# Kernel tuning notes

Measured on AMD Instinct MI355X. Metric: run time of the kernel, lower is better.

The kernel has to match this reference:

```python
import jax, jax.numpy as jnp
import numpy as np
from jax import lax

B, CIN, IMG, K = 128, 3, 112, 7
C = 1024      # hidden_channels * channel_dilation
HID = 512     # hidden_channels
HW = (IMG // K) ** 2  # 256 patches
EPS = 1e-5


def _prelu(x, a):
    return jnp.where(x > 0, x, a * x)


def _bn(x, g, b):
    # BatchNorm2d with track_running_stats=False: always uses batch stats
    m = x.mean(axis=(0, 2, 3), keepdims=True)
    v = x.var(axis=(0, 2, 3), keepdims=True)
    return (x - m) * lax.rsqrt(v + EPS) * g[None, :, None, None] + b[None, :, None, None]


def setup_inputs() -> dict:
    key = jax.random.key(0)
    ks = jax.random.split(key, 16)
    d = {
        'x':  jax.random.normal(ks[0], (B, CIN, IMG, IMG), jnp.float32),
        'w0': jax.random.normal(ks[1], (C, CIN, K, K), jnp.float32) * 0.05,
        'b0': jax.random.normal(ks[2], (C,), jnp.float32) * 0.01,
        'a0': jnp.full((1,), 0.25, jnp.float32),
    }
    for i in range(1, 4):
        kw, kb = jax.random.split(jax.random.fold_in(key, i))
        d[f'w{i}'] = jax.random.normal(kw, (C, C), jnp.float32) * 0.02
        d[f'b{i}'] = jax.random.normal(kb, (C,), jnp.float32) * 0.01
        d[f'g{i}'] = jnp.ones((C,), jnp.float32)
        d[f'bt{i}'] = jnp.zeros((C,), jnp.float32)
        d[f'p{i}'] = jnp.full((1,), 0.25, jnp.float32)
    d['pos'] = jax.random.normal(ks[3], (1, HW, C), jnp.float32)
    d['am'] = jnp.full((1,), 0.25, jnp.float32)
    d['wm'] = jax.random.normal(ks[4], (HID, C), jnp.float32) * 0.03
    d['bm'] = jax.random.normal(ks[5], (HID,), jnp.float32) * 0.01
    pkeys = jax.random.split(ks[6], B)
    d['perm'] = jax.vmap(lambda k: jax.random.permutation(k, HW))(pkeys).astype(jnp.int32)
    return d


def reference(x, w0, b0, a0,
              w1, b1, g1, bt1, p1,
              w2, b2, g2, bt2, p2,
              w3, b3, g3, bt3, p3,
              pos, am, wm, bm, perm):
    # patch-embed conv: stride = kernel_size -> [B, C, 16, 16]
    h = lax.conv_general_dilated(x, w0, (K, K), 'VALID',
                                 dimension_numbers=('NCHW', 'OIHW', 'NCHW'))
    h = _prelu(h + b0[None, :, None, None], a0)
    for w, b, g, bt, p in ((w1, b1, g1, bt1, p1),
                           (w2, b2, g2, bt2, p2),
                           (w3, b3, g3, bt3, p3)):
        h = jnp.einsum('bchw,dc->bdhw', h, w) + b[None, :, None, None]  # 1x1 conv
        h = _prelu(_bn(h, g, bt), p)
    Bn, Cn, Hn, Wn = h.shape
    enc = h.reshape(Bn, Cn, Hn * Wn).transpose(0, 2, 1)  # [B, HW, C]
    enc = enc + pos                                      # private: add pos embedding
    enc = _prelu(enc, am) @ wm.T + bm                    # mixer -> [B, HW, HID]
    # private: per-sample token permutation (single batched gather)
    return jnp.take_along_axis(enc, perm[:, :, None], axis=1)
```

## Files before the change

### kernel.cpp

```cpp
#include <hip/hip_runtime.h>
#include <hip/hip_bf16.h>
#include <stdint.h>


typedef __attribute__((ext_vector_type(8))) short bf16x8;
typedef __attribute__((ext_vector_type(4))) float f32x4;

__device__ __forceinline__ float bf2f(uint32_t u) {
  union { uint32_t i; float f; } v; v.i = u << 16; return v.f;
}
__device__ __forceinline__ ushort f2bf(float f) {
  union { float f; uint32_t i; } v; v.f = f;
  uint32_t i = v.i;
  return (ushort)((i + 0x7FFFu + ((i >> 16) & 1u)) >> 16);
}

template<int EPI, int XB, int K, int DOUT>
__global__ void __launch_bounds__(512, 2)
gemm_kernel(const ushort* __restrict__ A, const ushort* __restrict__ Bw,
            const float* __restrict__ bias, const float* __restrict__ alpha,
            void* __restrict__ outp, float* __restrict__ part,
            const int* __restrict__ inv)
{
  __shared__ __align__(16) ushort At[2][256 * 64];
  __shared__ __align__(16) ushort Bt[2][256 * 64];
  const int tid  = threadIdx.x;
  const int lane = tid & 63;
  const int wid  = tid >> 6;
  const int wm   = wid >> 2;
  const int wn   = wid & 3;

  const int s = blockIdx.x;
  const int j = s >> 3;
  const int x = j & ((1 << XB) - 1);
  const int y = ((j >> XB) << 3) | (s & 7);
  const int t0 = y << 8;
  const int d0 = x << 8;

  f32x4 acc[8][4] = {};

  const int swz = (((lane >> 4) ^ (lane & 7)) << 4);
  const char* LA0 = (const char*)&At[0][0] + ((((wm << 7) + (lane & 15))) << 7) + swz;
  const char* LA1 = (const char*)&At[0][0] + ((((wm << 7) + (lane & 15))) << 7) + (swz ^ 64);
  const char* LB0 = (const char*)&Bt[0][0] + ((((wn << 6) + (lane & 15))) << 7) + swz;
  const char* LB1 = (const char*)&Bt[0][0] + ((((wn << 6) + (lane & 15))) << 7) + (swz ^ 64);

  const int lrow8 = lane >> 3;
  const int csrc  = (lane & 7) ^ lrow8;
  const ushort* gAw = A  + (size_t)(t0 + (wid << 4) + lrow8) * K + (csrc << 3);
  const ushort* gBw = Bw + (size_t)(d0 + (wid << 4) + lrow8) * K + (csrc << 3);
  char* stA = (char*)&At[0][0] + (wid << 11);
  char* stB = (char*)&Bt[0][0] + (wid << 11);

#define STAGE_A(T, BUF, H) do {                                                          \
    __builtin_amdgcn_global_load_lds(                                                    \
      (const __attribute__((address_space(1))) uint32_t*)(gAw + (size_t)((H)*128)*K + ((size_t)(T) << 6)),     \
      (__attribute__((address_space(3))) uint32_t*)(stA + (BUF)*32768 + (H)*16384), 16, 0, 0);                  \
    __builtin_amdgcn_global_load_lds(                                                    \
      (const __attribute__((address_space(1))) uint32_t*)(gAw + (size_t)((H)*128+8)*K + ((size_t)(T) << 6)),   \
      (__attribute__((address_space(3))) uint32_t*)(stA + (BUF)*32768 + (H)*16384 + 1024), 16, 0, 0);           \
  } while (0)
#define STAGE_B(T, BUF, H) do {                                                          \
    __builtin_amdgcn_global_load_lds(                                                    \
      (const __attribute__((address_space(1))) uint32_t*)(gBw + (size_t)((H)*128)*K + ((size_t)(T) << 6)),     \
      (__attribute__((address_space(3))) uint32_t*)(stB + (BUF)*32768 + (H)*16384), 16, 0, 0);                  \
    __builtin_amdgcn_global_load_lds(                                                    \
      (const __attribute__((address_space(1))) uint32_t*)(gBw + (size_t)((H)*128+8)*K + ((size_t)(T) << 6)),   \
      (__attribute__((address_space(3))) uint32_t*)(stB + (BUF)*32768 + (H)*16384 + 1024), 16, 0, 0);           \
  } while (0)

#define RD_A(dst, BASE, CUR, MH) do {                                                    \
    dst[0] = *(const bf16x8*)((BASE) + (CUR)*32768 + (MH)*8192 + 0);                     \
    dst[1] = *(const bf16x8*)((BASE) + (CUR)*32768 + (MH)*8192 + 2048);                  \
    dst[2] = *(const bf16x8*)((BASE) + (CUR)*32768 + (MH)*8192 + 4096);                  \
    dst[3] = *(const bf16x8*)((BASE) + (CUR)*32768 + (MH)*8192 + 6144);                  \
  } while (0)
#define RD_B(dst, BASE, CUR) do {                                                        \
    dst[0] = *(const bf16x8*)((BASE) + (CUR)*32768 + 0);                                 \
    dst[1] = *(const bf16x8*)((BASE) + (CUR)*32768 + 2048);                              \
    dst[2] = *(const bf16x8*)((BASE) + (CUR)*32768 + 4096);                              \
    dst[3] = *(const bf16x8*)((BASE) + (CUR)*32768 + 6144);                              \
  } while (0)
#define MFMA16(AF, BF, MH) do {                                                          \
    __builtin_amdgcn_s_setprio(1);                                                       \
    _Pragma("unroll")                                                                    \
    for (int m_ = 0; m_ < 4; ++m_)                                                       \
      _Pragma("unroll")                                                                  \
      for (int n_ = 0; n_ < 4; ++n_)                                                     \
        acc[((MH) << 2) + m_][n_] = __builtin_amdgcn_mfma_f32_16x16x32_bf16(             \
            AF[m_], BF[n_], acc[((MH) << 2) + m_][n_], 0, 0, 0);                         \
    __builtin_amdgcn_s_setprio(0);                                                       \
  } while (0)

#define TILE_BODY(T, CUR, HN1, HN2) do {                                                 \
                               \
    if (HN1) { asm volatile("s_waitcnt vmcnt(4)" ::: "memory"); }                        \
    else     { asm volatile("s_waitcnt vmcnt(0)" ::: "memory"); }                        \
    __builtin_amdgcn_s_barrier();                                                        \
                                                                                \
    RD_A(aX, LA0, CUR, 0);                                                               \
    RD_B(b0f, LB0, CUR);                                                                 \
    if (HN1) { STAGE_A((T) + 1, (CUR) ^ 1, 0); STAGE_A((T) + 1, (CUR) ^ 1, 1); }         \
    MFMA16(aX, b0f, 0);                                                                  \
                                                                                \
    RD_A(aY, LA0, CUR, 1);                                                               \
    MFMA16(aY, b0f, 1);                                                                  \
                                                                                \
    RD_A(aX, LA1, CUR, 0);                                                               \
    RD_B(b1f, LB1, CUR);                                                                 \
    MFMA16(aX, b1f, 0);                                                                  \
                       \
    __builtin_amdgcn_s_barrier();                                                        \
    if (HN2) { STAGE_B((T) + 2, CUR, 0); STAGE_B((T) + 2, CUR, 1); }                     \
                                  \
    RD_A(aY, LA1, CUR, 1);                                                               \
    MFMA16(aY, b1f, 1);                                                                  \
  } while (0)

  constexpr int NT = K >> 6;

  STAGE_A(0, 0, 0); STAGE_A(0, 0, 1);
  STAGE_B(0, 0, 0); STAGE_B(0, 0, 1);
  STAGE_B(1, 1, 0); STAGE_B(1, 1, 1);

  bf16x8 aX[4], aY[4], b0f[4], b1f[4];

#pragma unroll 1
  for (int tp = 0; tp < NT; tp += 2) {
    const bool m1 = (tp + 2 < NT);
    TILE_BODY(tp,     0, true, m1);
    TILE_BODY(tp + 1, 1, m1, m1);
  }

  float bs[4];
#pragma unroll
  for (int n = 0; n < 4; ++n) bs[n] = bias[d0 + (wn << 6) + (n << 4) + (lane & 15)];
  float a0v = (EPI == 0) ? alpha[0] : 0.0f;
  float sA[4] = {0.f, 0.f, 0.f, 0.f}, s2A[4] = {0.f, 0.f, 0.f, 0.f};

#pragma unroll
  for (int m = 0; m < 8; ++m) {
#pragma unroll
    for (int r = 0; r < 4; ++r) {
      int row = t0 + (wm << 7) + (m << 4) + ((lane >> 4) << 2) + r;
      int orow = (EPI == 2) ? ((row & ~255) | inv[row]) : row;
#pragma unroll
      for (int n = 0; n < 4; ++n) {
        int d = d0 + (wn << 6) + (n << 4) + (lane & 15);
        float v = acc[m][n][r] + bs[n];
        if (EPI == 0) v = v > 0.f ? v : a0v * v;
        if (EPI == 1) { sA[n] += v; s2A[n] += v * v; }
        if (EPI == 2) ((float*)outp)[(size_t)orow * DOUT + d] = v;
        else          ((ushort*)outp)[(size_t)row * DOUT + d] = f2bf(v);
      }
    }
  }

  if (EPI == 1) {
    float2* sm = (float2*)&At[0][0];
    int slot = (wm << 2) | (lane >> 4);
    __syncthreads();
#pragma unroll
    for (int n = 0; n < 4; ++n) {
      int c = (wn << 6) + (n << 4) + (lane & 15);
      sm[slot * 256 + c] = make_float2(sA[n], s2A[n]);
    }
    __syncthreads();
    if (tid < 256) {
      float ss = 0.f, ss2 = 0.f;
      for (int q = 0; q < 8; ++q) {
        float2 v = sm[q * 256 + tid];
        ss += v.x; ss2 += v.y;
      }
      part[(size_t)y * 2048 + d0 + tid]        = ss;
      part[(size_t)y * 2048 + 1024 + d0 + tid] = ss2;
    }
  }
#undef STAGE_A
#undef STAGE_B
#undef RD_A
#undef RD_B
#undef MFMA16
#undef TILE_BODY
}

__global__ void bnfold_kernel(const float* __restrict__ part, const float* __restrict__ g,
                              const float* __restrict__ bt, float* __restrict__ scsh) {
  int d = (blockIdx.x << 8) + threadIdx.x;
  float s = 0.f, s2 = 0.f;
  for (int j = 0; j < 128; ++j) { s += part[j * 2048 + d]; s2 += part[j * 2048 + 1024 + d]; }
  float mean = s * (1.f / 32768.f);
  float var  = s2 * (1.f / 32768.f) - mean * mean;
  float sc = g[d] * rsqrtf(var + 1e-5f);
  scsh[d] = sc;
  scsh[1024 + d] = bt[d] - mean * sc;
}

template<bool MIX>
__global__ void bnact_kernel(ushort* __restrict__ Y, const float* __restrict__ scsh,
                             const float* __restrict__ p, const float* __restrict__ pos,
                             const float* __restrict__ am) {
  size_t i = (((size_t)blockIdx.x << 8) + threadIdx.x) << 3;
  int d = (int)(i & 1023);
  float pp = p[0];
  float aa = MIX ? am[0] : 0.f;
  float pv[8];
  if (MIX) {
    int prow = (int)((i >> 10) & 255);
    const float4* pb = (const float4*)(pos + ((size_t)prow << 10) + d);
    float4 pA = pb[0], pB = pb[1];
    pv[0]=pA.x; pv[1]=pA.y; pv[2]=pA.z; pv[3]=pA.w;
    pv[4]=pB.x; pv[5]=pB.y; pv[6]=pB.z; pv[7]=pB.w;
  }
  uint4 raw = *(const uint4*)(Y + i);
  uint32_t w[4] = {raw.x, raw.y, raw.z, raw.w};
  uint32_t o[4];
#pragma unroll
  for (int q = 0; q < 4; ++q) {
    int dd = d + q * 2;
    float v0 = bf2f(w[q] & 0xFFFFu) * scsh[dd]     + scsh[1024 + dd];
    float v1 = bf2f(w[q] >> 16)     * scsh[dd + 1] + scsh[1024 + dd + 1];
    v0 = v0 > 0.f ? v0 : pp * v0;
    v1 = v1 > 0.f ? v1 : pp * v1;
    if (MIX) {
      v0 += pv[2 * q];     v1 += pv[2 * q + 1];
      v0 = v0 > 0.f ? v0 : aa * v0;
      v1 = v1 > 0.f ? v1 : aa * v1;
    }
    o[q] = (uint32_t)f2bf(v0) | ((uint32_t)f2bf(v1) << 16);
  }
  *(uint4*)(Y + i) = make_uint4(o[0], o[1], o[2], o[3]);
}

__global__ void invperm_kernel(const int* __restrict__ perm, int* __restrict__ inv) {
  int t = (blockIdx.x << 8) + threadIdx.x;
  inv[(t & ~255) + perm[t]] = t & 255;
}

__global__ void f2b_kernel(const float* __restrict__ in, ushort* __restrict__ out, int n) {
  int i = (blockIdx.x << 8) + threadIdx.x;
  if (i < n) out[i] = f2bf(in[i]);
}

__global__ void padw0_kernel(const float* __restrict__ w0, ushort* __restrict__ o) {
  int d = blockIdx.x, j = threadIdx.x;
  o[d * 256 + j] = (j < 147) ? f2bf(w0[d * 147 + j]) : (ushort)0;
}

__global__ void im2col_kernel(const float* __restrict__ x, ushort* __restrict__ P) {
  int t = blockIdx.x;
  int j = threadIdx.x;
  ushort v = 0;
  if (j < 147) {
    int b = t >> 8, pidx = t & 255;
    int pi = pidx >> 4, pj = pidx & 15;
    int cin = j / 49, rem = j - cin * 49;
    int dy = rem / 7, dx = rem - dy * 7;
    v = f2bf(x[(size_t)(b * 3 + cin) * 12544 + (size_t)(pi * 7 + dy) * 112 + (pj * 7 + dx)]);
  }
  P[(size_t)t * 256 + j] = v;
}

extern "C" void kernel_launch(void* const* d_in, const int* in_sizes, int n_in,
                              void* d_out, int out_size, void* d_ws, size_t ws_size,
                              hipStream_t stream) {
  const float* x   = (const float*)d_in[0];
  const float* w0  = (const float*)d_in[1];
  const float* b0  = (const float*)d_in[2];
  const float* a0  = (const float*)d_in[3];
  const float* w1  = (const float*)d_in[4];
  const float* b1  = (const float*)d_in[5];
  const float* g1  = (const float*)d_in[6];
  const float* bt1 = (const float*)d_in[7];
  const float* p1  = (const float*)d_in[8];
  const float* w2  = (const float*)d_in[9];
  const float* b2  = (const float*)d_in[10];
  const float* g2  = (const float*)d_in[11];
  const float* bt2 = (const float*)d_in[12];
  const float* p2  = (const float*)d_in[13];
  const float* w3  = (const float*)d_in[14];
  const float* b3  = (const float*)d_in[15];
  const float* g3  = (const float*)d_in[16];
  const float* bt3 = (const float*)d_in[17];
  const float* p3  = (const float*)d_in[18];
  const float* pos = (const float*)d_in[19];
  const float* am  = (const float*)d_in[20];
  const float* wm  = (const float*)d_in[21];
  const float* bm  = (const float*)d_in[22];
  const int*  perm = (const int*)d_in[23];

  char* ws = (char*)d_ws;
  ushort* B0   = (ushort*)ws;
  ushort* B1   = (ushort*)(ws + 67108864);
  float*  part = (float*)(ws + 134217728);
  float*  scsh = (float*)(ws + 134217728 + 2097152);
  int*    inv  = (int*)  (ws + 134217728 + 2097152 + 8192);
  ushort* wbuf = (ushort*)(ws + 134217728 + 2097152 + 8192 + 131072);

  invperm_kernel<<<dim3(128), dim3(256), 0, stream>>>(perm, inv);
  im2col_kernel<<<dim3(32768), dim3(256), 0, stream>>>(x, B1);
  padw0_kernel<<<dim3(1024), dim3(256), 0, stream>>>(w0, wbuf);

  gemm_kernel<0, 2, 256, 1024><<<dim3(512), dim3(512), 0, stream>>>(
      B1, wbuf, b0, a0, (void*)B0, nullptr, nullptr);

  f2b_kernel<<<dim3(4096), dim3(256), 0, stream>>>(w1, wbuf, 1048576);
  gemm_kernel<1, 2, 1024, 1024><<<dim3(512), dim3(512), 0, stream>>>(
      B0, wbuf, b1, nullptr, (void*)B1, part, nullptr);
  bnfold_kernel<<<dim3(4), dim3(256), 0, stream>>>(part, g1, bt1, scsh);
  bnact_kernel<false><<<dim3(16384), dim3(256), 0, stream>>>(B1, scsh, p1, nullptr, nullptr);

  f2b_kernel<<<dim3(4096), dim3(256), 0, stream>>>(w2, wbuf, 1048576);
  gemm_kernel<1, 2, 1024, 1024><<<dim3(512), dim3(512), 0, stream>>>(
      B1, wbuf, b2, nullptr, (void*)B0, part, nullptr);
  bnfold_kernel<<<dim3(4), dim3(256), 0, stream>>>(part, g2, bt2, scsh);
  bnact_kernel<false><<<dim3(16384), dim3(256), 0, stream>>>(B0, scsh, p2, nullptr, nullptr);

  f2b_kernel<<<dim3(4096), dim3(256), 0, stream>>>(w3, wbuf, 1048576);
  gemm_kernel<1, 2, 1024, 1024><<<dim3(512), dim3(512), 0, stream>>>(
      B0, wbuf, b3, nullptr, (void*)B1, part, nullptr);
  bnfold_kernel<<<dim3(4), dim3(256), 0, stream>>>(part, g3, bt3, scsh);
  bnact_kernel<true><<<dim3(16384), dim3(256), 0, stream>>>(B1, scsh, p3, pos, am);

  f2b_kernel<<<dim3(2048), dim3(256), 0, stream>>>(wm, wbuf, 524288);
  gemm_kernel<2, 1, 1024, 512><<<dim3(256), dim3(512), 0, stream>>>(
      B1, wbuf, bm, nullptr, d_out, nullptr, inv);
}
```

Before: 394.2 us.

## Fuse BatchNorm apply and PReLU into the next GEMM's A-operand load

Removes the three standalone bnact passes and instead applies the BN scale/shift, PReLU, and (for the last layer) the positional add and mixer PReLU while loading the A tile of the following GEMM. A tiles now go global→registers→transform→LDS instead of direct global_load_lds. This saves a full read and write of the 64MB bf16 activation per layer. In exchange it adds VGPR pressure, per-element ALU inside the GEMM main loop, and extra waitcnt synchronisation that can stall the MFMA pipeline.

```diff
diff --git a/kernel.cpp b/kernel.cpp
--- a/kernel.cpp
+++ b/kernel.cpp
@@ -15,12 +15,33 @@
   return (ushort)((i + 0x7FFFu + ((i >> 16) & 1u)) >> 16);
 }
 
-template<int EPI, int XB, int K, int DOUT>
+template<int PRE>
+__device__ __forceinline__ bf16x8 bnproc(bf16x8 r, float4 sc0, float4 sc1,
+                                         float4 sh0, float4 sh1,
+                                         float4 pv0, float4 pv1,
+                                         float pp, float aa) {
+  float sca[8] = {sc0.x, sc0.y, sc0.z, sc0.w, sc1.x, sc1.y, sc1.z, sc1.w};
+  float sha[8] = {sh0.x, sh0.y, sh0.z, sh0.w, sh1.x, sh1.y, sh1.z, sh1.w};
+  float pva[8] = {pv0.x, pv0.y, pv0.z, pv0.w, pv1.x, pv1.y, pv1.z, pv1.w};
+  bf16x8 o;
+#pragma unroll
+  for (int j = 0; j < 8; ++j) {
+    float v = bf2f((uint32_t)(ushort)r[j]) * sca[j] + sha[j];
+    v = v > 0.f ? v : pp * v;
+    if (PRE == 2) { v += pva[j]; v = v > 0.f ? v : aa * v; }
+    o[j] = (short)f2bf(v);
+  }
+  return o;
+}
+
+template<int EPI, int PRE, int XB, int K, int DOUT>
 __global__ void __launch_bounds__(512, 2)
 gemm_kernel(const ushort* __restrict__ A, const ushort* __restrict__ Bw,
             const float* __restrict__ bias, const float* __restrict__ alpha,
             void* __restrict__ outp, float* __restrict__ part,
-            const int* __restrict__ inv)
+            const int* __restrict__ inv, const float* __restrict__ scshp,
+            const float* __restrict__ pA, const float* __restrict__ posp,
+            const float* __restrict__ pam)
 {
   __shared__ __align__(16) ushort At[2][256 * 64];
   __shared__ __align__(16) ushort Bt[2][256 * 64];
@@ -47,10 +68,19 @@
 
   const int lrow8 = lane >> 3;
   const int csrc  = (lane & 7) ^ lrow8;
-  const ushort* gAw = A  + (size_t)(t0 + (wid << 4) + lrow8) * K + (csrc << 3);
-  const ushort* gBw = Bw + (size_t)(d0 + (wid << 4) + lrow8) * K + (csrc << 3);
-  char* stA = (char*)&At[0][0] + (wid << 11);
-  char* stB = (char*)&Bt[0][0] + (wid << 11);
+  const int kq    = csrc << 3;
+  const int rbase = (wid << 4) + lrow8;
+  const ushort* gAw = A  + (size_t)(t0 + rbase) * K + kq;
+  const ushort* gBw = Bw + (size_t)(d0 + rbase) * K + kq;
+  char* stA  = (char*)&At[0][0] + (wid << 11);
+  char* stB  = (char*)&Bt[0][0] + (wid << 11);
+  char* stAw = (char*)&At[0][0] + (wid << 11) + (lane << 4);
+
+  float ppA = (PRE >= 1) ? pA[0]  : 0.f;
+  float aaM = (PRE == 2) ? pam[0] : 0.f;
+
+  bf16x8 ar0, ar1, ar2, ar3;
+  float4 sc0_, sc1_, sh0_, sh1_;
 
 #define STAGE_A(T, BUF, H) do {                                                          \
     __builtin_amdgcn_global_load_lds(                                                    \
@@ -67,6 +97,48 @@
     __builtin_amdgcn_global_load_lds(                                                    \
       (const __attribute__((address_space(1))) uint32_t*)(gBw + (size_t)((H)*128+8)*K + ((size_t)(T) << 6)),   \
       (__attribute__((address_space(3))) uint32_t*)(stB + (BUF)*32768 + (H)*16384 + 1024), 16, 0, 0);           \
+  } while (0)
+
+#define ISSUE_A_REG(T) do {                                                              \
+    const ushort* pa_ = gAw + ((size_t)(T) << 6);                                        \
+    ar0 = *(const bf16x8*)(pa_);                                                         \
+    ar1 = *(const bf16x8*)(pa_ + (size_t)8 * K);                                         \
+    ar2 = *(const bf16x8*)(pa_ + (size_t)128 * K);                                       \
+    ar3 = *(const bf16x8*)(pa_ + (size_t)136 * K);                                       \
+    const float* sp_ = scshp + ((T) << 6) + kq;                                          \
+    sc0_ = *(const float4*)(sp_);        sc1_ = *(const float4*)(sp_ + 4);               \
+    sh0_ = *(const float4*)(sp_ + 1024); sh1_ = *(const float4*)(sp_ + 1028);            \
+  } while (0)
+
+#define WRITE_A_REG(T, BUF) do {                                                         \
+    bf16x8 w0_, w1_, w2_, w3_;                                                           \
+    if constexpr (PRE == 2) {                                                            \
+      const float* pb_ = posp + ((T) << 6) + kq;                                         \
+      float4 q00 = *(const float4*)(pb_ + (size_t)(rbase      ) * 1024);                 \
+      float4 q01 = *(const float4*)(pb_ + (size_t)(rbase      ) * 1024 + 4);             \
+      float4 q10 = *(const float4*)(pb_ + (size_t)(rbase +   8) * 1024);                 \
+      float4 q11 = *(const float4*)(pb_ + (size_t)(rbase +   8) * 1024 + 4);             \
+      float4 q20 = *(const float4*)(pb_ + (size_t)(rbase + 128) * 1024);                 \
+      float4 q21 = *(const float4*)(pb_ + (size_t)(rbase + 128) * 1024 + 4);             \
+      float4 q30 = *(const float4*)(pb_ + (size_t)(rbase + 136) * 1024);                 \
+      float4 q31 = *(const float4*)(pb_ + (size_t)(rbase + 136) * 1024 + 4);             \
+      w0_ = bnproc<2>(ar0, sc0_, sc1_, sh0_, sh1_, q00, q01, ppA, aaM);                  \
+      w1_ = bnproc<2>(ar1, sc0_, sc1_, sh0_, sh1_, q10, q11, ppA, aaM);                  \
+      w2_ = bnproc<2>(ar2, sc0_, sc1_, sh0_, sh1_, q20, q21, ppA, aaM);                  \
+      w3_ = bnproc<2>(ar3, sc0_, sc1_, sh0_, sh1_, q30, q31, ppA, aaM);                  \
+    } else {                                                                             \
+      float4 z_ = make_float4(0.f, 0.f, 0.f, 0.f);                                       \
+      w0_ = bnproc<1>(ar0, sc0_, sc1_, sh0_, sh1_, z_, z_, ppA, 0.f);                    \
+      w1_ = bnproc<1>(ar1, sc0_, sc1_, sh0_, sh1_, z_, z_, ppA, 0.f);                    \
+      w2_ = bnproc<1>(ar2, sc0_, sc1_, sh0_, sh1_, z_, z_, ppA, 0.f);                    \
+      w3_ = bnproc<1>(ar3, sc0_, sc1_, sh0_, sh1_, z_, z_, ppA, 0.f);                    \
+    }                                                                                    \
+    char* d_ = stAw + (BUF) * 32768;                                                     \
+    *(bf16x8*)(d_ + 0)     = w0_;                                                        \
+    *(bf16x8*)(d_ + 1024)  = w1_;                                                        \
+    *(bf16x8*)(d_ + 16384) = w2_;                                                        \
+    *(bf16x8*)(d_ + 17408) = w3_;                                                        \
+    asm volatile("s_waitcnt lgkmcnt(0)" ::: "memory");                                   \
   } while (0)
 
 #define RD_A(dst, BASE, CUR, MH) do {                                                    \
@@ -93,14 +165,16 @@
   } while (0)
 
 #define TILE_BODY(T, CUR, HN1, HN2) do {                                                 \
-                               \
     if (HN1) { asm volatile("s_waitcnt vmcnt(4)" ::: "memory"); }                        \
     else     { asm volatile("s_waitcnt vmcnt(0)" ::: "memory"); }                        \
     __builtin_amdgcn_s_barrier();                                                        \
                                                                                 \
     RD_A(aX, LA0, CUR, 0);                                                               \
     RD_B(b0f, LB0, CUR);                                                                 \
-    if (HN1) { STAGE_A((T) + 1, (CUR) ^ 1, 0); STAGE_A((T) + 1, (CUR) ^ 1, 1); }         \
+    if (HN1) {                                                                           \
+      if constexpr (PRE == 0) { STAGE_A((T) + 1, (CUR) ^ 1, 0); STAGE_A((T) + 1, (CUR) ^ 1, 1); } \
+      else ISSUE_A_REG((T) + 1);                                                         \
+    }                                                                                    \
     MFMA16(aX, b0f, 0);                                                                  \
                                                                                 \
     RD_A(aY, LA0, CUR, 1);                                                               \
@@ -109,17 +183,28 @@
     RD_A(aX, LA1, CUR, 0);                                                               \
     RD_B(b1f, LB1, CUR);                                                                 \
     MFMA16(aX, b1f, 0);                                                                  \
-                       \
+                                       \
     __builtin_amdgcn_s_barrier();                                                        \
     if (HN2) { STAGE_B((T) + 2, CUR, 0); STAGE_B((T) + 2, CUR, 1); }                     \
-                                  \
+    if constexpr (PRE >= 1) {                                                            \
+      if (HN2)      { asm volatile("s_waitcnt vmcnt(4)" ::: "memory"); }                 \
+      else if (HN1) { asm volatile("s_waitcnt vmcnt(0)" ::: "memory"); }                 \
+      if (HN1) WRITE_A_REG((T) + 1, (CUR) ^ 1);                                          \
+    }                                                                                    \
+                                                                                \
     RD_A(aY, LA1, CUR, 1);                                                               \
     MFMA16(aY, b1f, 1);                                                                  \
   } while (0)
 
   constexpr int NT = K >> 6;
 
-  STAGE_A(0, 0, 0); STAGE_A(0, 0, 1);
+  if constexpr (PRE == 0) {
+    STAGE_A(0, 0, 0); STAGE_A(0, 0, 1);
+  } else {
+    ISSUE_A_REG(0);
+    asm volatile("s_waitcnt vmcnt(0)" ::: "memory");
+    WRITE_A_REG(0, 0);
+  }
   STAGE_B(0, 0, 0); STAGE_B(0, 0, 1);
   STAGE_B(1, 1, 0); STAGE_B(1, 1, 1);
 
@@ -178,6 +263,8 @@
   }
 #undef STAGE_A
 #undef STAGE_B
+#undef ISSUE_A_REG
+#undef WRITE_A_REG
 #undef RD_A
 #undef RD_B
 #undef MFMA16
@@ -194,42 +281,6 @@
   float sc = g[d] * rsqrtf(var + 1e-5f);
   scsh[d] = sc;
   scsh[1024 + d] = bt[d] - mean * sc;
-}
-
-template<bool MIX>
-__global__ void bnact_kernel(ushort* __restrict__ Y, const float* __restrict__ scsh,
-                             const float* __restrict__ p, const float* __restrict__ pos,
-                             const float* __restrict__ am) {
-  size_t i = (((size_t)blockIdx.x << 8) + threadIdx.x) << 3;
-  int d = (int)(i & 1023);
-  float pp = p[0];
-  float aa = MIX ? am[0] : 0.f;
-  float pv[8];
-  if (MIX) {
-    int prow = (int)((i >> 10) & 255);
-    const float4* pb = (const float4*)(pos + ((size_t)prow << 10) + d);
-    float4 pA = pb[0], pB = pb[1];
-    pv[0]=pA.x; pv[1]=pA.y; pv[2]=pA.z; pv[3]=pA.w;
-    pv[4]=pB.x; pv[5]=pB.y; pv[6]=pB.z; pv[7]=pB.w;
-  }
-  uint4 raw = *(const uint4*)(Y + i);
-  uint32_t w[4] = {raw.x, raw.y, raw.z, raw.w};
-  uint32_t o[4];
-#pragma unroll
-  for (int q = 0; q < 4; ++q) {
-    int dd = d + q * 2;
-    float v0 = bf2f(w[q] & 0xFFFFu) * scsh[dd]     + scsh[1024 + dd];
-    float v1 = bf2f(w[q] >> 16)     * scsh[dd + 1] + scsh[1024 + dd + 1];
-    v0 = v0 > 0.f ? v0 : pp * v0;
-    v1 = v1 > 0.f ? v1 : pp * v1;
-    if (MIX) {
-      v0 += pv[2 * q];     v1 += pv[2 * q + 1];
-      v0 = v0 > 0.f ? v0 : aa * v0;
-      v1 = v1 > 0.f ? v1 : aa * v1;
-    }
-    o[q] = (uint32_t)f2bf(v0) | ((uint32_t)f2bf(v1) << 16);
-  }
-  *(uint4*)(Y + i) = make_uint4(o[0], o[1], o[2], o[3]);
 }
 
 __global__ void invperm_kernel(const int* __restrict__ perm, int* __restrict__ inv) {
@@ -301,28 +352,25 @@
   im2col_kernel<<<dim3(32768), dim3(256), 0, stream>>>(x, B1);
   padw0_kernel<<<dim3(1024), dim3(256), 0, stream>>>(w0, wbuf);
 
-  gemm_kernel<0, 2, 256, 1024><<<dim3(512), dim3(512), 0, stream>>>(
-      B1, wbuf, b0, a0, (void*)B0, nullptr, nullptr);
+  gemm_kernel<0, 0, 2, 256, 1024><<<dim3(512), dim3(512), 0, stream>>>(
+      B1, wbuf, b0, a0, (void*)B0, nullptr, nullptr, nullptr, nullptr, nullptr, nullptr);
 
   f2b_kernel<<<dim3(4096), dim3(256), 0, stream>>>(w1, wbuf, 1048576);
-  gemm_kernel<1, 2, 1024, 1024><<<dim3(512), dim3(512), 0, stream>>>(
-      B0, wbuf, b1, nullptr, (void*)B1, part, nullptr);
+  gemm_kernel<1, 0, 2, 1024, 1024><<<dim3(512), dim3(512), 0, stream>>>(
+      B0, wbuf, b1, nullptr, (void*)B1, part, nullptr, nullptr, nullptr, nullptr, nullptr);
   bnfold_kernel<<<dim3(4), dim3(256), 0, stream>>>(part, g1, bt1, scsh);
-  bnact_kernel<false><<<dim3(16384), dim3(256), 0, stream>>>(B1, scsh, p1, nullptr, nullptr);
 
   f2b_kernel<<<dim3(4096), dim3(256), 0, stream>>>(w2, wbuf, 1048576);
-  gemm_kernel<1, 2, 1024, 1024><<<dim3(512), dim3(512), 0, stream>>>(
-      B1, wbuf, b2, nullptr, (void*)B0, part, nullptr);
+  gemm_kernel<1, 1, 2, 1024, 1024><<<dim3(512), dim3(512), 0, stream>>>(
+      B1, wbuf, b2, nullptr, (void*)B0, part, nullptr, scsh, p1, nullptr, nullptr);
   bnfold_kernel<<<dim3(4), dim3(256), 0, stream>>>(part, g2, bt2, scsh);
-  bnact_kernel<false><<<dim3(16384), dim3(256), 0, stream>>>(B0, scsh, p2, nullptr, nullptr);
 
   f2b_kernel<<<dim3(4096), dim3(256), 0, stream>>>(w3, wbuf, 1048576);
-  gemm_kernel<1, 2, 1024, 1024><<<dim3(512), dim3(512), 0, stream>>>(
-      B0, wbuf, b3, nullptr, (void*)B1, part, nullptr);
+  gemm_kernel<1, 1, 2, 1024, 1024><<<dim3(512), dim3(512), 0, stream>>>(
+      B0, wbuf, b3, nullptr, (void*)B1, part, nullptr, scsh, p2, nullptr, nullptr);
   bnfold_kernel<<<dim3(4), dim3(256), 0, stream>>>(part, g3, bt3, scsh);
-  bnact_kernel<true><<<dim3(16384), dim3(256), 0, stream>>>(B1, scsh, p3, pos, am);
 
   f2b_kernel<<<dim3(2048), dim3(256), 0, stream>>>(wm, wbuf, 524288);
-  gemm_kernel<2, 1, 1024, 512><<<dim3(256), dim3(512), 0, stream>>>(
-      B1, wbuf, bm, nullptr, d_out, nullptr, inv);
-}
+  gemm_kernel<2, 2, 1, 1024, 512><<<dim3(256), dim3(512), 0, stream>>>(
+      B1, wbuf, bm, nullptr, d_out, nullptr, inv, scsh, p3, pos, am);
+}
```

After: 481.6 us. 22.2% more time.
